# Kernel tuning notes

Measured on AMD Instinct MI355X. Metric: run time of the kernel, lower is better.

Reference implementation:

```python
import jax, jax.numpy as jnp
import numpy as np

NUM_TAPS = 4096
LOWCUT, HIGHCUT, FS = 30.0, 1024.0, 4096
B, C, T = 8, 4, 131072


def firwin_bandpass(num_taps, low, high, fs):
    # Replicates scipy.signal.firwin(numtaps, [low, high], pass_zero=False, fs=fs)
    nyq = fs / 2.0
    l, h = low / nyq, high / nyq
    m = np.arange(num_taps) - (num_taps - 1) / 2.0
    h_ideal = h * np.sinc(h * m) - l * np.sinc(l * m)  # ideal bandpass
    hk = h_ideal * np.hamming(num_taps)  # symmetric Hamming (scipy default)
    fc = (l + h) / 2.0  # scale frequency = band midpoint
    hk = hk / np.sum(hk * np.cos(np.pi * m * fc))
    return hk.astype(np.float32)


def _fir_conv(x, kernel):
    # Depthwise 'same' cross-correlation matching torch conv1d(padding='same').
    # x: [B, C, T], kernel: [K]
    Cc = x.shape[1]
    K = kernel.shape[0]
    left, right = (K - 1) // 2, K // 2  # torch 'same' asymmetric pad for even K
    w = jnp.broadcast_to(kernel[None, None, :], (Cc, 1, K))  # [C,1,K] depthwise
    return jax.lax.conv_general_dilated(
        x, w, window_strides=(1,), padding=[(left, right)],
        dimension_numbers=('NCH', 'OIH', 'NCH'), feature_group_count=Cc)


def setup_inputs() -> dict:
    key = jax.random.key(0)
    x = jax.random.normal(key, (B, C, T), dtype=jnp.float32)
    kernel = jnp.asarray(firwin_bandpass(NUM_TAPS, LOWCUT, HIGHCUT, FS))
    return {"x": x, "kernel": kernel}


def reference(x, kernel):
    pad = NUM_TAPS // 2
    xp = jnp.pad(x, ((0, 0), (0, 0), (pad, pad)), mode='reflect')
    y = _fir_conv(xp, kernel)
    # zero-phase: filter time-reversed signal, reverse back
    y = _fir_conv(y[..., ::-1], kernel)[..., ::-1]
    return y[..., pad:-pad]
```

## Files before the change

kernel.cpp:

```cpp
#include <hip/hip_runtime.h>


#define T_LEN   131072
#define XE_LEN  139776
#define XE_U4   (XE_LEN / 8)
#define NCHUNK  312
#define QQ      72
#define SCH     8
#define NCH     9

typedef float  f32x4  __attribute__((ext_vector_type(4)));
typedef __bf16 bf16x8 __attribute__((ext_vector_type(8)));

#define WS_KZ   0
#define WS_G    49152
#define WS_AHI  81920
#define WS_XE   401408
#define WS_END  9347072

__device__ __forceinline__ void gload_lds16(const uint4* g, uint4* lds) {
  __builtin_amdgcn_global_load_lds(
      (const __attribute__((address_space(1))) unsigned int*)g,
      (__attribute__((address_space(3))) unsigned int*)lds, 16, 0, 0);
}

__global__ void k_autocorr(const float* __restrict__ k,
                           const float* __restrict__ kz,
                           float* __restrict__ g) {
  int s = blockIdx.x * 256 + threadIdx.x;
  int i0 = blockIdx.y * 256;
  const float* kk  = k + i0;
  const float* kzs = kz + (8191 - s) + i0;
  float a0 = 0.f, a1 = 0.f, a2 = 0.f, a3 = 0.f;
  #pragma unroll 4
  for (int i = 0; i < 256; i += 4) {
    float4 kv = *(const float4*)(kk + i);
    float4 zv;
    __builtin_memcpy(&zv, kzs + i, 16);
    a0 = fmaf(kv.x, zv.x, a0);
    a1 = fmaf(kv.y, zv.y, a1);
    a2 = fmaf(kv.z, zv.z, a2);
    a3 = fmaf(kv.w, zv.w, a3);
  }
  atomicAdd(&g[s], (a0 + a1) + (a2 + a3));
}

__global__ void k_build_afrag(const float* __restrict__ g,
                              __bf16* __restrict__ Ahi) {
  int P = blockIdx.x;
  int t = threadIdx.x;
  int l = t >> 2;
  int jj0 = (t & 3) * 2;
  int q = l >> 4, i = l & 15;
  int p = P - 24;
  #pragma unroll
  for (int u = 0; u < 2; ++u) {
    int jj = jj0 + u;
    int s = 32 * p + 8 * q + jj - i;
    float val = (s >= 0 && s <= 8190) ? g[s] : 0.0f;
    Ahi[P * 512 + l * 8 + jj] = (__bf16)val;
  }
}

__global__ void k_build_xe(const float* __restrict__ x, __bf16* __restrict__ xe,
                           const float* __restrict__ k, float* __restrict__ kz,
                           float* __restrict__ g) {
  if (blockIdx.y == 0) {
    int m = blockIdx.x * 256 + threadIdx.x;
    if (m < 12288) {
      int i = m - 4096;
      kz[m] = (i >= 0 && i < 4096) ? k[i] : 0.0f;
    }
    if (m < 8192) g[m] = 0.0f;
  }
  int e0 = (blockIdx.x * 256 + threadIdx.x) * 8;
  int row = blockIdx.y;
  if (e0 >= XE_LEN) return;
  const float* xr = x + (size_t)row * T_LEN;
  int v0 = e0 - 4095;
  bf16x8 outv;
  if (v0 >= 0 && v0 <= T_LEN - 8) {
    float4 f0, f1;
    __builtin_memcpy(&f0, xr + v0, 16);
    __builtin_memcpy(&f1, xr + v0 + 4, 16);
    outv[0] = (__bf16)f0.x; outv[1] = (__bf16)f0.y;
    outv[2] = (__bf16)f0.z; outv[3] = (__bf16)f0.w;
    outv[4] = (__bf16)f1.x; outv[5] = (__bf16)f1.y;
    outv[6] = (__bf16)f1.z; outv[7] = (__bf16)f1.w;
  } else {
    #pragma unroll
    for (int u = 0; u < 8; ++u) {
      int v = v0 + u;
      float val = 0.0f;
      if (v >= -2048 && v < T_LEN + 2048) {
        int v2 = v < 0 ? -v : v;
        v2 = v2 >= T_LEN ? 2 * T_LEN - 2 - v2 : v2;
        val = xr[v2];
      }
      outv[u] = (__bf16)val;
    }
  }
  ((uint4*)(xe + (size_t)row * XE_LEN))[e0 >> 3] =
      __builtin_bit_cast(uint4, outv);
}

__global__ __launch_bounds__(512, 4) void k_fir_mfma(
    const uint4* __restrict__ xeu, const uint4* __restrict__ Ahi,
    float* __restrict__ out) {
  __shared__ uint4 sbB[4096];

  const int tid = threadIdx.x;
  const int w   = tid >> 6;
  const int l   = tid & 63;
  const int q   = l >> 4;
  const int n   = l & 15;
  const int qh  = w & 3;
  const int rg  = w >> 2;

  const int orig = blockIdx.x;
  const int flat = (orig & 7) * 64 + (orig >> 3);
  const int bx   = flat & 127;
  const int by   = flat >> 7;

  const int t0     = bx << 10;
  const int brbase = by << 3;
  const int wrbase = brbase + (rg << 2);
  const int Qbeg   = qh * QQ;
  const int lofs   = q + 2 * n;

  const uint4* gbase = xeu + (size_t)wrbase * XE_U4 + (t0 >> 3) + 4 * Qbeg + l;
  uint4* sw = sbB + (w << 9);

  f32x4 acc[4][4];
  #pragma unroll
  for (int r = 0; r < 4; ++r)
    #pragma unroll
    for (int m = 0; m < 4; ++m) acc[r][m] = (f32x4){0.f, 0.f, 0.f, 0.f};

  #pragma unroll
  for (int r = 0; r < 4; ++r)
    gload_lds16(gbase + (size_t)r * XE_U4, sw + (r << 6));
  asm volatile("s_waitcnt vmcnt(0)" ::: "memory");

  int buf = 0;
  for (int ch = 0; ch < NCH; ++ch) {
    if (ch + 1 < NCH) {
      uint4* dst = sw + ((buf ^ 1) << 8);
      const uint4* src = gbase + ((ch + 1) << 5);
      #pragma unroll
      for (int r = 0; r < 4; ++r)
        gload_lds16(src + (size_t)r * XE_U4, dst + (r << 6));
    }

    const uint4* bw = sw + (buf << 8) + lofs;
    #pragma unroll 2
    for (int Qr = 0; Qr < SCH; ++Qr) {
      const int Q = Qbeg + (ch << 3) + Qr;
      bf16x8 A[4];
      #pragma unroll
      for (int mt = 0; mt < 4; ++mt)
        A[mt] = __builtin_bit_cast(bf16x8, Ahi[(Q + 24 - 8 * mt) * 64 + l]);
      bf16x8 Bv[4];
      #pragma unroll
      for (int r = 0; r < 4; ++r)
        Bv[r] = __builtin_bit_cast(bf16x8, bw[(r << 6) + 4 * Qr]);
      __builtin_amdgcn_s_setprio(1);
      #pragma unroll
      for (int r = 0; r < 4; ++r)
        #pragma unroll
        for (int mt = 0; mt < 4; ++mt)
          acc[r][mt] = __builtin_amdgcn_mfma_f32_16x16x32_bf16(
              A[mt], Bv[r], acc[r][mt], 0, 0, 0);
      __builtin_amdgcn_s_setprio(0);
    }

    if (ch + 1 < NCH) {
      asm volatile("s_waitcnt vmcnt(0)" ::: "memory");
      buf ^= 1;
    }
  }

  __syncthreads();
  float* C = (float*)sbB;
  const int co = (q << 2) + (n << 4);
  #pragma unroll
  for (int ph = 0; ph < 4; ++ph) {
    const int mt = (qh + ph) & 3;
    float* cp = C + ((rg << 2) << 10) + (mt << 8) + co;
    if (ph == 0) {
      #pragma unroll
      for (int r = 0; r < 4; ++r)
        *(f32x4*)(cp + (r << 10)) = acc[r][mt];
    } else {
      #pragma unroll
      for (int r = 0; r < 4; ++r) {
        f32x4 v = *(f32x4*)(cp + (r << 10));
        v += acc[r][mt];
        *(f32x4*)(cp + (r << 10)) = v;
      }
    }
    __syncthreads();
  }

  #pragma unroll
  for (int u = 0; u < 4; ++u) {
    const int idx = tid + (u << 9);
    f32x4 v = ((f32x4*)C)[idx];
    const int row = idx >> 8;
    const int tc  = (idx & 255) << 2;
    *(f32x4*)(out + (size_t)(brbase + row) * T_LEN + t0 + tc) = v;
  }
}

extern "C" void kernel_launch(void* const* d_in, const int* in_sizes, int n_in,
                              void* d_out, int out_size, void* d_ws, size_t ws_size,
                              hipStream_t stream) {
  const float* x = (const float*)d_in[0];
  const float* k = (const float*)d_in[1];
  float* out = (float*)d_out;
  char* ws = (char*)d_ws;
  if (ws_size < (size_t)WS_END) return;

  float*  kz  = (float*)(ws + WS_KZ);
  float*  g   = (float*)(ws + WS_G);
  __bf16* Ahi = (__bf16*)(ws + WS_AHI);
  __bf16* xe  = (__bf16*)(ws + WS_XE);

  k_build_xe<<<dim3((XE_LEN / 8 + 255) / 256, 32), dim3(256), 0, stream>>>(
      x, xe, k, kz, g);
  k_autocorr<<<dim3(32, 16), dim3(256), 0, stream>>>(k, kz, g);
  k_build_afrag<<<dim3(NCHUNK), dim3(256), 0, stream>>>(g, Ahi);
  k_fir_mfma<<<dim3(512), dim3(512), 0, stream>>>(
      (const uint4*)xe, (const uint4*)Ahi, out);
}
```

Measured before the change: 163.4 us.

## Software-pipeline A-fragment global loads with register double buffering in MFMA loop

The inner Q loop is fully unrolled, and the A fragments for the next step are loaded from global memory into a second register set while the current step's MFMAs run, so their latency is hidden. The next chunk's LDS prefetch is also issued after the first two steps instead of at the start of each chunk. This adds roughly 16 VGPRs for the extra A buffer, which may pressure occupancy under the 512x4 launch bounds. The s_waitcnt vmcnt(0) now also waits on the outstanding A prefetch.

After: 201.9 us. 1.24x slower.

```diff
diff --git a/kernel.cpp b/kernel.cpp
--- a/kernel.cpp
+++ b/kernel.cpp
@@ -6,7 +6,6 @@
 #define XE_U4   (XE_LEN / 8)
 #define NCHUNK  312
 #define QQ      72
-#define SCH     8
 #define NCH     9
 
 typedef float  f32x4  __attribute__((ext_vector_type(4)));
@@ -104,6 +103,31 @@
       __builtin_bit_cast(uint4, outv);
 }
 
+#define STEP(Qr, AC, AN)                                                   \
+  {                                                                        \
+    bf16x8 Bv[4];                                                          \
+    _Pragma("unroll")                                                      \
+    for (int r = 0; r < 4; ++r)                                            \
+      Bv[r] = __builtin_bit_cast(bf16x8, bw[(r << 6) + 4 * (Qr)]);         \
+    if ((Qr) < 7) {                          \
+      _Pragma("unroll")                                                    \
+      for (int mt = 0; mt < 4; ++mt)                                       \
+        AN[mt] = __builtin_bit_cast(bf16x8, Acb[((Qr) + 1 - 8 * mt) * 64]);\
+    } else if (ch + 1 < NCH) {              \
+      _Pragma("unroll")                                                    \
+      for (int mt = 0; mt < 4; ++mt)                                       \
+        AN[mt] = __builtin_bit_cast(bf16x8, Acb[(8 - 8 * mt) * 64]);       \
+    }                                                                      \
+    __builtin_amdgcn_s_setprio(1);                                         \
+    _Pragma("unroll")                                                      \
+    for (int r = 0; r < 4; ++r)                                            \
+      _Pragma("unroll")                                                    \
+      for (int mt = 0; mt < 4; ++mt)                                       \
+        acc[r][mt] = __builtin_amdgcn_mfma_f32_16x16x32_bf16(              \
+            AC[mt], Bv[r], acc[r][mt], 0, 0, 0);                           \
+    __builtin_amdgcn_s_setprio(0);                                         \
+  }
+
 __global__ __launch_bounds__(512, 4) void k_fir_mfma(
     const uint4* __restrict__ xeu, const uint4* __restrict__ Ahi,
     float* __restrict__ out) {
@@ -130,6 +154,7 @@
 
   const uint4* gbase = xeu + (size_t)wrbase * XE_U4 + (t0 >> 3) + 4 * Qbeg + l;
   uint4* sw = sbB + (w << 9);
+  const bf16x8* Ahi8 = (const bf16x8*)Ahi;
 
   f32x4 acc[4][4];
   #pragma unroll
@@ -140,10 +165,20 @@
   #pragma unroll
   for (int r = 0; r < 4; ++r)
     gload_lds16(gbase + (size_t)r * XE_U4, sw + (r << 6));
+  bf16x8 A0[4], A1[4];
+  #pragma unroll
+  for (int mt = 0; mt < 4; ++mt)
+    A0[mt] = __builtin_bit_cast(bf16x8, Ahi8[(size_t)(Qbeg + 24 - 8 * mt) * 64 + l]);
   asm volatile("s_waitcnt vmcnt(0)" ::: "memory");
 
   int buf = 0;
   for (int ch = 0; ch < NCH; ++ch) {
+    const uint4*  bw  = sw + (buf << 8) + lofs;
+    const bf16x8* Acb = Ahi8 + (size_t)(Qbeg + ch * 8 + 24) * 64 + l;
+
+    STEP(0, A0, A1)
+    STEP(1, A1, A0)
+
     if (ch + 1 < NCH) {
       uint4* dst = sw + ((buf ^ 1) << 8);
       const uint4* src = gbase + ((ch + 1) << 5);
@@ -152,27 +187,12 @@
         gload_lds16(src + (size_t)r * XE_U4, dst + (r << 6));
     }
 
-    const uint4* bw = sw + (buf << 8) + lofs;
-    #pragma unroll 2
-    for (int Qr = 0; Qr < SCH; ++Qr) {
-      const int Q = Qbeg + (ch << 3) + Qr;
-      bf16x8 A[4];
-      #pragma unroll
-      for (int mt = 0; mt < 4; ++mt)
-        A[mt] = __builtin_bit_cast(bf16x8, Ahi[(Q + 24 - 8 * mt) * 64 + l]);
-      bf16x8 Bv[4];
-      #pragma unroll
-      for (int r = 0; r < 4; ++r)
-        Bv[r] = __builtin_bit_cast(bf16x8, bw[(r << 6) + 4 * Qr]);
-      __builtin_amdgcn_s_setprio(1);
-      #pragma unroll
-      for (int r = 0; r < 4; ++r)
-        #pragma unroll
-        for (int mt = 0; mt < 4; ++mt)
-          acc[r][mt] = __builtin_amdgcn_mfma_f32_16x16x32_bf16(
-              A[mt], Bv[r], acc[r][mt], 0, 0, 0);
-      __builtin_amdgcn_s_setprio(0);
-    }
+    STEP(2, A0, A1)
+    STEP(3, A1, A0)
+    STEP(4, A0, A1)
+    STEP(5, A1, A0)
+    STEP(6, A0, A1)
+    STEP(7, A1, A0)
 
     if (ch + 1 < NCH) {
       asm volatile("s_waitcnt vmcnt(0)" ::: "memory");
```

## Keep Toeplitz A-fragments in a register ring and load from compact padded g

Applied to the files above, without the earlier changes.

Replaces the precomputed per-fragment Ahi table with a compact padded bf16 copy of the autocorrelation (two copies offset by one element for lane alignment), built by a smaller kernel. The MFMA kernel now keeps a rotating ring of 32 A-fragments in registers. Each of the four m-tiles reuses a fragment loaded several sub-steps earlier, so only one new global load is issued per Q step instead of four, and the chunk loop is fully unrolled via a macro. The cost is many more VGPRs, so launch bounds drop from 4 to 2 waves per SIMD, which lowers occupancy and latency hiding.

Result: faster. 149.7 us (-8.4%).

```diff
diff --git a/kernel.cpp b/kernel.cpp
--- a/kernel.cpp
+++ b/kernel.cpp
@@ -4,18 +4,17 @@
 #define T_LEN   131072
 #define XE_LEN  139776
 #define XE_U4   (XE_LEN / 8)
-#define NCHUNK  312
 #define QQ      72
-#define SCH     8
 #define NCH     9
+#define GP_STRIDE 24576
 
 typedef float  f32x4  __attribute__((ext_vector_type(4)));
 typedef __bf16 bf16x8 __attribute__((ext_vector_type(8)));
 
 #define WS_KZ   0
 #define WS_G    49152
-#define WS_AHI  81920
-#define WS_XE   401408
+#define WS_GP   81920
+#define WS_XE   131072
 #define WS_END  9347072
 
 __device__ __forceinline__ void gload_lds16(const uint4* g, uint4* lds) {
@@ -45,21 +44,14 @@
   atomicAdd(&g[s], (a0 + a1) + (a2 + a3));
 }
 
-__global__ void k_build_afrag(const float* __restrict__ g,
-                              __bf16* __restrict__ Ahi) {
-  int P = blockIdx.x;
-  int t = threadIdx.x;
-  int l = t >> 2;
-  int jj0 = (t & 3) * 2;
-  int q = l >> 4, i = l & 15;
-  int p = P - 24;
-  #pragma unroll
-  for (int u = 0; u < 2; ++u) {
-    int jj = jj0 + u;
-    int s = 32 * p + 8 * q + jj - i;
-    float val = (s >= 0 && s <= 8190) ? g[s] : 0.0f;
-    Ahi[P * 512 + l * 8 + jj] = (__bf16)val;
-  }
+__global__ void k_build_gpad(const float* __restrict__ g,
+                             char* __restrict__ gp) {
+  int idx = blockIdx.x * 256 + threadIdx.x;
+  int e = idx - 1024;
+  float v = (e >= 0 && e <= 8190) ? g[e] : 0.0f;
+  __bf16 b = (__bf16)v;
+  *(__bf16*)(gp + 2 * idx) = b;
+  *(__bf16*)(gp + GP_STRIDE + 2 + 2 * idx) = b;
 }
 
 __global__ void k_build_xe(const float* __restrict__ x, __bf16* __restrict__ xe,
@@ -104,8 +96,47 @@
       __builtin_bit_cast(uint4, outv);
 }
 
-__global__ __launch_bounds__(512, 4) void k_fir_mfma(
-    const uint4* __restrict__ xeu, const uint4* __restrict__ Ahi,
+#define CHUNK(CH, BUF, GA, GB, GC, GD, DO_STAGE)                           \
+  {                                                                        \
+    if (DO_STAGE) {                                                        \
+      uint4* dst = sw + ((BUF ^ 1) << 8);                                  \
+      const uint4* src = gbase + (((CH) + 1) << 5);                        \
+      _Pragma("unroll")                                                    \
+      for (int r = 0; r < 4; ++r)                                          \
+        gload_lds16(src + (size_t)r * XE_U4, dst + (r << 6));              \
+    }                                                                      \
+    const uint4* bw = sw + ((BUF) << 8) + lofs;                            \
+    _Pragma("unroll")                                                      \
+    for (int Qr = 0; Qr < 8; ++Qr) {                                       \
+      bf16x8 Bv[4];                                                        \
+      _Pragma("unroll")                                                    \
+      for (int r = 0; r < 4; ++r)                                          \
+        Bv[r] = __builtin_bit_cast(bf16x8, bw[(r << 6) + 4 * Qr]);         \
+      bf16x8 a3 = GA[Qr], a2 = GB[Qr], a1 = GC[Qr], a0 = GD[Qr];           \
+      uint4 tmp;                                                           \
+      __builtin_memcpy(&tmp,                                               \
+          laneA + ((size_t)(Qbeg + (CH) * 8 + 32 + Qr) << 6), 16);         \
+      GA[Qr] = __builtin_bit_cast(bf16x8, tmp);                            \
+      __builtin_amdgcn_s_setprio(1);                                       \
+      _Pragma("unroll")                                                    \
+      for (int r = 0; r < 4; ++r) {                                        \
+        acc[r][0] = __builtin_amdgcn_mfma_f32_16x16x32_bf16(a0, Bv[r],     \
+                                                            acc[r][0], 0, 0, 0); \
+        acc[r][1] = __builtin_amdgcn_mfma_f32_16x16x32_bf16(a1, Bv[r],     \
+                                                            acc[r][1], 0, 0, 0); \
+        acc[r][2] = __builtin_amdgcn_mfma_f32_16x16x32_bf16(a2, Bv[r],     \
+                                                            acc[r][2], 0, 0, 0); \
+        acc[r][3] = __builtin_amdgcn_mfma_f32_16x16x32_bf16(a3, Bv[r],     \
+                                                            acc[r][3], 0, 0, 0); \
+      }                                                                    \
+      __builtin_amdgcn_s_setprio(0);                                       \
+    }                                                                      \
+    if (DO_STAGE)                                                          \
+      asm volatile("s_waitcnt vmcnt(0)" ::: "memory");                     \
+  }
+
+__global__ __launch_bounds__(512, 2) void k_fir_mfma(
+    const uint4* __restrict__ xeu, const char* __restrict__ gpad,
     float* __restrict__ out) {
   __shared__ uint4 sbB[4096];
 
@@ -131,54 +162,42 @@
   const uint4* gbase = xeu + (size_t)wrbase * XE_U4 + (t0 >> 3) + 4 * Qbeg + l;
   uint4* sw = sbB + (w << 9);
 
+  const char* laneA = gpad + ((n & 1) ? (GP_STRIDE + 2) : 0)
+                      + 16 * q - 2 * n + 512;
+
   f32x4 acc[4][4];
   #pragma unroll
   for (int r = 0; r < 4; ++r)
     #pragma unroll
     for (int m = 0; m < 4; ++m) acc[r][m] = (f32x4){0.f, 0.f, 0.f, 0.f};
 
+  bf16x8 G0[8], G1[8], G2[8], G3[8];
+  #pragma unroll
+  for (int j = 0; j < 8; ++j) {
+    uint4 u0, u1, u2, u3;
+    __builtin_memcpy(&u0, laneA + ((size_t)(Qbeg + j) << 6), 16);
+    __builtin_memcpy(&u1, laneA + ((size_t)(Qbeg + 8 + j) << 6), 16);
+    __builtin_memcpy(&u2, laneA + ((size_t)(Qbeg + 16 + j) << 6), 16);
+    __builtin_memcpy(&u3, laneA + ((size_t)(Qbeg + 24 + j) << 6), 16);
+    G0[j] = __builtin_bit_cast(bf16x8, u0);
+    G1[j] = __builtin_bit_cast(bf16x8, u1);
+    G2[j] = __builtin_bit_cast(bf16x8, u2);
+    G3[j] = __builtin_bit_cast(bf16x8, u3);
+  }
   #pragma unroll
   for (int r = 0; r < 4; ++r)
     gload_lds16(gbase + (size_t)r * XE_U4, sw + (r << 6));
   asm volatile("s_waitcnt vmcnt(0)" ::: "memory");
 
-  int buf = 0;
-  for (int ch = 0; ch < NCH; ++ch) {
-    if (ch + 1 < NCH) {
-      uint4* dst = sw + ((buf ^ 1) << 8);
-      const uint4* src = gbase + ((ch + 1) << 5);
-      #pragma unroll
-      for (int r = 0; r < 4; ++r)
-        gload_lds16(src + (size_t)r * XE_U4, dst + (r << 6));
-    }
-
-    const uint4* bw = sw + (buf << 8) + lofs;
-    #pragma unroll 2
-    for (int Qr = 0; Qr < SCH; ++Qr) {
-      const int Q = Qbeg + (ch << 3) + Qr;
-      bf16x8 A[4];
-      #pragma unroll
-      for (int mt = 0; mt < 4; ++mt)
-        A[mt] = __builtin_bit_cast(bf16x8, Ahi[(Q + 24 - 8 * mt) * 64 + l]);
-      bf16x8 Bv[4];
-      #pragma unroll
-      for (int r = 0; r < 4; ++r)
-        Bv[r] = __builtin_bit_cast(bf16x8, bw[(r << 6) + 4 * Qr]);
-      __builtin_amdgcn_s_setprio(1);
-      #pragma unroll
-      for (int r = 0; r < 4; ++r)
-        #pragma unroll
-        for (int mt = 0; mt < 4; ++mt)
-          acc[r][mt] = __builtin_amdgcn_mfma_f32_16x16x32_bf16(
-              A[mt], Bv[r], acc[r][mt], 0, 0, 0);
-      __builtin_amdgcn_s_setprio(0);
-    }
-
-    if (ch + 1 < NCH) {
-      asm volatile("s_waitcnt vmcnt(0)" ::: "memory");
-      buf ^= 1;
-    }
-  }
+  CHUNK(0, 0, G0, G1, G2, G3, 1)
+  CHUNK(1, 1, G1, G2, G3, G0, 1)
+  CHUNK(2, 0, G2, G3, G0, G1, 1)
+  CHUNK(3, 1, G3, G0, G1, G2, 1)
+  CHUNK(4, 0, G0, G1, G2, G3, 1)
+  CHUNK(5, 1, G1, G2, G3, G0, 1)
+  CHUNK(6, 0, G2, G3, G0, G1, 1)
+  CHUNK(7, 1, G3, G0, G1, G2, 1)
+  CHUNK(8, 0, G0, G1, G2, G3, 0)
 
   __syncthreads();
   float* C = (float*)sbB;
@@ -221,15 +240,15 @@
   char* ws = (char*)d_ws;
   if (ws_size < (size_t)WS_END) return;
 
-  float*  kz  = (float*)(ws + WS_KZ);
-  float*  g   = (float*)(ws + WS_G);
-  __bf16* Ahi = (__bf16*)(ws + WS_AHI);
-  __bf16* xe  = (__bf16*)(ws + WS_XE);
+  float* kz = (float*)(ws + WS_KZ);
+  float* g  = (float*)(ws + WS_G);
+  char*  gp = ws + WS_GP;
+  __bf16* xe = (__bf16*)(ws + WS_XE);
 
   k_build_xe<<<dim3((XE_LEN / 8 + 255) / 256, 32), dim3(256), 0, stream>>>(
       x, xe, k, kz, g);
   k_autocorr<<<dim3(32, 16), dim3(256), 0, stream>>>(k, kz, g);
-  k_build_afrag<<<dim3(NCHUNK), dim3(256), 0, stream>>>(g, Ahi);
+  k_build_gpad<<<dim3(44), dim3(256), 0, stream>>>(g, gp);
   k_fir_mfma<<<dim3(512), dim3(512), 0, stream>>>(
-      (const uint4*)xe, (const uint4*)Ahi, out);
-}
+      (const uint4*)xe, gp, out);
+}
```
